# Kernel tuning notes

Measured on AMD Instinct MI355X. Metric: run time of the kernel, lower is better.

## Reference

```python
import jax, jax.numpy as jnp
import numpy as np

B, S, H, I, E, K = 2, 512, 1024, 4096, 8, 2
LN_EPS = 1e-5


def setup_inputs() -> dict:
    key = jax.random.key(0)
    ks = jax.random.split(key, 5)
    sc = 0.02  # init scale for weights
    return {
        "hidden_states": jax.random.normal(ks[0], (B, S, H), jnp.float32),
        "ln_w": jnp.ones((H,), jnp.float32),
        "ln_b": jnp.zeros((H,), jnp.float32),
        "Wr": jax.random.normal(ks[1], (E, H), jnp.float32) * sc,  # router [out=E, in=H]
        "br": jnp.zeros((E,), jnp.float32),
        "W1": jax.random.normal(ks[2], (E, I, H), jnp.float32) * sc,  # dense1 per expert [out=I, in=H]
        "b1": jnp.zeros((E, I), jnp.float32),
        "W2": jax.random.normal(ks[3], (E, H, I), jnp.float32) * sc,  # dense2 per expert [out=H, in=I]
        "b2": jnp.zeros((E, H), jnp.float32),
    }


def reference(hidden_states, ln_w, ln_b, Wr, br, W1, b1, W2, b2):
    # Eval mode: no jitter noise, no dropout.
    residual = hidden_states
    mu = jnp.mean(hidden_states, axis=-1, keepdims=True)
    var = jnp.mean(jnp.square(hidden_states - mu), axis=-1, keepdims=True)
    x = (hidden_states - mu) * jax.lax.rsqrt(var + LN_EPS) * ln_w + ln_b  # [B,S,H]

    logits = jnp.einsum("bsh,eh->bse", x, Wr) + br  # [B,S,E]
    topw, topi = jax.lax.top_k(logits, K)  # [B,S,K]
    topw = jax.nn.softmax(topw, axis=-1)
    # Combine weights per expert (top-k indices are distinct, so scatter == first-match)
    combine = jnp.sum(jax.nn.one_hot(topi, E, dtype=x.dtype) * topw[..., None], axis=-2)  # [B,S,E]

    # Dense per-expert FFN (reference form of gather-FFN-scatter); combine zeros out unselected experts
    a = jax.nn.gelu(jnp.einsum("bsh,eih->bsei", x, W1) + b1, approximate=False)  # [B,S,E,I]
    y = jnp.einsum("bsei,ehi->bseh", a, W2) + b2  # [B,S,E,H]
    out = residual + jnp.einsum("bse,bseh->bsh", combine, y)

    probs = jax.nn.softmax(logits, axis=-1)
    usage = jnp.mean(probs, axis=(0, 1))  # [E]
    balance_loss = E * jnp.sum(usage * usage) - 1.0
    return out, balance_loss
```

## Files before the change

### kernel.cpp

```cpp
#include <hip/hip_runtime.h>
#include <hip/hip_bf16.h>
#include <math.h>
#include <stdint.h>

#define T_TOK 1024
#define H_DIM 1024
#define I_DIM 4096
#define E_NUM 8
#define NSLOT (2 * T_TOK)
#define WELEM 33554432

typedef __attribute__((ext_vector_type(8))) short bf16x8;
typedef __attribute__((ext_vector_type(4))) float f32x4;

#define MFMA_BF16(a, b, c) __builtin_amdgcn_mfma_f32_16x16x32_bf16(a, b, c, 0, 0, 0)

__device__ __forceinline__ short f2bf(float f) {
  union { float f; unsigned u; } x; x.f = f;
  unsigned r = (x.u + 0x7fffu + ((x.u >> 16) & 1u)) >> 16;
  return (short)r;
}
__device__ __forceinline__ int pack2bf(float a, float b) {
  return ((int)(unsigned short)f2bf(a)) | (((int)f2bf(b)) << 16);
}

typedef __attribute__((address_space(3))) unsigned int as3_u32;
typedef const __attribute__((address_space(1))) unsigned int as1_u32c;
__device__ __forceinline__ void glds16(const void* g, void* l) {
  __builtin_amdgcn_global_load_lds((as1_u32c*)g, (as3_u32*)l, 16, 0, 0);
}

union BBCast { int4 i4; bf16x8 v; };

__global__ __launch_bounds__(256) void k_ln_router(
    const float* __restrict__ x, const float* __restrict__ ln_w,
    const float* __restrict__ ln_b, const float* __restrict__ Wr,
    const float* __restrict__ br,
    short* __restrict__ xln, int* __restrict__ sel_e, float* __restrict__ sel_w,
    float* __restrict__ probs, float* __restrict__ out) {
  const int t = blockIdx.x;
  const int tid = threadIdx.x;
  const int lane = tid & 63, wid = tid >> 6;
  __shared__ float sx[H_DIM];
  __shared__ float redS[8];
  __shared__ float slog[E_NUM];

  float4 v = ((const float4*)(x + (size_t)t * H_DIM))[tid];
  ((float4*)(out + (size_t)t * H_DIM))[tid] = v;
  float s = v.x + v.y + v.z + v.w;
  float ss = v.x * v.x + v.y * v.y + v.z * v.z + v.w * v.w;
  for (int o = 32; o > 0; o >>= 1) { s += __shfl_down(s, o); ss += __shfl_down(ss, o); }
  if (lane == 0) { redS[wid] = s; redS[4 + wid] = ss; }
  __syncthreads();
  float st = redS[0] + redS[1] + redS[2] + redS[3];
  float sst = redS[4] + redS[5] + redS[6] + redS[7];
  float mu = st * (1.0f / H_DIM);
  float var = sst * (1.0f / H_DIM) - mu * mu;
  float rs = rsqrtf(var + 1e-5f);

  float4 lw = ((const float4*)ln_w)[tid];
  float4 lb = ((const float4*)ln_b)[tid];
  float4 xn;
  xn.x = (v.x - mu) * rs * lw.x + lb.x;
  xn.y = (v.y - mu) * rs * lw.y + lb.y;
  xn.z = (v.z - mu) * rs * lw.z + lb.z;
  xn.w = (v.w - mu) * rs * lw.w + lb.w;
  sx[4 * tid + 0] = xn.x; sx[4 * tid + 1] = xn.y;
  sx[4 * tid + 2] = xn.z; sx[4 * tid + 3] = xn.w;
  short4 s4;
  s4.x = f2bf(xn.x); s4.y = f2bf(xn.y); s4.z = f2bf(xn.z); s4.w = f2bf(xn.w);
  ((short4*)(xln + (size_t)t * H_DIM))[tid] = s4;
  __syncthreads();

  for (int e = 2 * wid; e < 2 * wid + 2; ++e) {
    float p = 0.f;
    for (int h = lane; h < H_DIM; h += 64) p += sx[h] * Wr[e * H_DIM + h];
    for (int o = 32; o > 0; o >>= 1) p += __shfl_down(p, o);
    if (lane == 0) slog[e] = p + br[e];
  }
  __syncthreads();

  if (tid == 0) {
    float lg[E_NUM];
    for (int e = 0; e < E_NUM; ++e) lg[e] = slog[e];
    int i0 = 0;
    for (int e = 1; e < E_NUM; ++e) if (lg[e] > lg[i0]) i0 = e;
    int i1 = (i0 == 0) ? 1 : 0;
    for (int e = 0; e < E_NUM; ++e) if (e != i0 && lg[e] > lg[i1]) i1 = e;
    float w1e = __expf(lg[i1] - lg[i0]);
    float den = 1.f + w1e;
    sel_e[2 * t] = i0; sel_w[2 * t] = 1.f / den;
    sel_e[2 * t + 1] = i1; sel_w[2 * t + 1] = w1e / den;
    float se = 0.f, pe[E_NUM];
    for (int e = 0; e < E_NUM; ++e) { pe[e] = __expf(lg[e] - lg[i0]); se += pe[e]; }
    float inv = 1.f / se;
    for (int e = 0; e < E_NUM; ++e) probs[t * E_NUM + e] = pe[e] * inv;
  }
}

__global__ __launch_bounds__(512) void k_route(
    const int* __restrict__ sel_e, const float* __restrict__ sel_w,
    const float* __restrict__ probs,
    int* __restrict__ counts, int* __restrict__ basep,
    int* __restrict__ tlist, int* __restrict__ sel_idx,
    float* __restrict__ wslot, float* __restrict__ loss_out) {
  const int wid = threadIdx.x >> 6;
  const int lane = threadIdx.x & 63;
  __shared__ int scnt[E_NUM];
  __shared__ float susage[E_NUM];

  int cnt = 0;
  for (int s0 = 0; s0 < NSLOT; s0 += 64) {
    int s = s0 + lane;
    bool m = (sel_e[s] == wid);
    unsigned long long mk = __ballot(m);
    int pre = __popcll(mk & ((1ULL << lane) - 1ULL));
    if (m) {
      int idx = cnt + pre;
      sel_idx[s] = idx;
      tlist[wid * T_TOK + idx] = s >> 1;
      wslot[wid * T_TOK + idx] = sel_w[s];
    }
    cnt += __popcll(mk);
  }
  if (lane == 0) scnt[wid] = cnt;

  float u = 0.f;
  for (int t = lane; t < T_TOK; t += 64) u += probs[t * E_NUM + wid];
  for (int o = 32; o > 0; o >>= 1) u += __shfl_down(u, o);
  if (lane == 0) susage[wid] = u * (1.0f / T_TOK);
  __syncthreads();

  if (threadIdx.x == 0) {
    int b = 0;
    for (int e = 0; e < E_NUM; ++e) { basep[e] = b; counts[e] = scnt[e]; b += scnt[e]; }
    float sq = 0.f;
    for (int e = 0; e < E_NUM; ++e) sq += susage[e] * susage[e];
    *loss_out = (float)E_NUM * sq - 1.0f;
  }
}

__global__ __launch_bounds__(256) void k_cvt(const float* __restrict__ src,
                                             short* __restrict__ dst, int n) {
  const int stride = gridDim.x * blockDim.x;
  for (int i = blockIdx.x * blockDim.x + threadIdx.x; i < (n >> 3); i += stride) {
    float4 a = ((const float4*)src)[2 * i];
    float4 b = ((const float4*)src)[2 * i + 1];
    int4 p;
    p.x = pack2bf(a.x, a.y); p.y = pack2bf(a.z, a.w);
    p.z = pack2bf(b.x, b.y); p.w = pack2bf(b.z, b.w);
    ((int4*)dst)[i] = p;
  }
}

__global__ __launch_bounds__(256) void k_ffn1(
    const short* __restrict__ xln, const short* __restrict__ W1b,
    const float* __restrict__ b1, const int* __restrict__ counts,
    const int* __restrict__ basep, const int* __restrict__ tlist,
    short* __restrict__ a_buf) {
  const int e = blockIdx.z;
  const int cnt = counts[e];
  const int m0 = blockIdx.y * 128;
  if (m0 >= cnt) return;
  const int n0 = blockIdx.x * 128;

  __shared__ __align__(16) short As[3][128 * 32];
  __shared__ __align__(16) short Bs[3][128 * 32];

  const int tid = threadIdx.x;
  const int lane = tid & 63, wid = tid >> 6;
  const int wr = wid >> 1, wc = wid & 1;
  const int fr = lane & 15, fq = lane >> 4;

  int r0 = m0 + (tid >> 2); if (r0 >= cnt) r0 = cnt - 1;
  int r1 = m0 + 64 + (tid >> 2); if (r1 >= cnt) r1 = cnt - 1;
  const short* ag0 = xln + (size_t)tlist[e * T_TOK + r0] * H_DIM + (tid & 3) * 8;
  const short* ag1 = xln + (size_t)tlist[e * T_TOK + r1] * H_DIM + (tid & 3) * 8;
  const short* bg0 = W1b + ((size_t)e * I_DIM + n0 + (tid >> 2)) * H_DIM + (tid & 3) * 8;
  const short* bg1 = bg0 + (size_t)64 * H_DIM;

  f32x4 acc[4][4];
#pragma unroll
  for (int i = 0; i < 4; ++i)
#pragma unroll
    for (int j = 0; j < 4; ++j) acc[i][j] = (f32x4)0.f;

#define STAGE(kk, buf)                                  \
  {                                                     \
    glds16(ag0 + (kk), &As[buf][tid * 8]);              \
    glds16(ag1 + (kk), &As[buf][(256 + tid) * 8]);      \
    glds16(bg0 + (kk), &Bs[buf][tid * 8]);              \
    glds16(bg1 + (kk), &Bs[buf][(256 + tid) * 8]);      \
  }

  STAGE(0, 0);
  STAGE(32, 1);

  const int KT = H_DIM / 32;
  for (int kt = 0; kt < KT; ++kt) {
    if (kt == KT - 1) {
      asm volatile("s_waitcnt vmcnt(0)" ::: "memory");
    } else {
      asm volatile("s_waitcnt vmcnt(4)" ::: "memory");
    }
    __builtin_amdgcn_s_barrier();
    if (kt + 2 < KT) STAGE((kt + 2) * 32, (kt + 2) % 3);
    const int cb = kt % 3;
    bf16x8 af[4], bb[4];
#pragma unroll
    for (int mi = 0; mi < 4; ++mi)
      af[mi] = *(const bf16x8*)&As[cb][(wr * 64 + mi * 16 + fr) * 32 + fq * 8];
#pragma unroll
    for (int ni = 0; ni < 4; ++ni)
      bb[ni] = *(const bf16x8*)&Bs[cb][(wc * 64 + ni * 16 + fr) * 32 + fq * 8];
#pragma unroll
    for (int mi = 0; mi < 4; ++mi)
#pragma unroll
      for (int ni = 0; ni < 4; ++ni)
        acc[mi][ni] = MFMA_BF16(af[mi], bb[ni], acc[mi][ni]);
  }
#undef STAGE

  const int slot0 = basep[e] + m0;
  float b1v[4];
#pragma unroll
  for (int ni = 0; ni < 4; ++ni)
    b1v[ni] = b1[e * I_DIM + n0 + wc * 64 + ni * 16 + fr];
#pragma unroll
  for (int mi = 0; mi < 4; ++mi)
#pragma unroll
    for (int j = 0; j < 4; ++j) {
      int r = wr * 64 + mi * 16 + fq * 4 + j;
      if (m0 + r < cnt) {
        size_t rowoff = (size_t)(slot0 + r) * I_DIM;
#pragma unroll
        for (int ni = 0; ni < 4; ++ni) {
          int colg = n0 + wc * 64 + ni * 16 + fr;
          float vv = acc[mi][ni][j] + b1v[ni];
          float g = 0.5f * vv * (1.0f + erff(vv * 0.70710678118654752f));
          a_buf[rowoff + colg] = f2bf(g);
        }
      }
    }
}

__global__ __launch_bounds__(256) void k_ffn2(
    const short* __restrict__ a_buf, const short* __restrict__ W2b,
    const float* __restrict__ b2, const int* __restrict__ counts,
    const int* __restrict__ basep, const int* __restrict__ tlist,
    const float* __restrict__ wslot, float* __restrict__ out) {
  const int z = blockIdx.z;
  const int e = z >> 2;
  const int kc = z & 3;
  const int CH = I_DIM / 4;
  const int cnt = counts[e];
  const int m0 = blockIdx.y * 128;
  if (m0 >= cnt) return;
  const int n0 = blockIdx.x * 128;

  __shared__ __align__(16) short As[3][128 * 32];
  __shared__ __align__(16) short Bs[3][128 * 32];

  const int tid = threadIdx.x;
  const int lane = tid & 63, wid = tid >> 6;
  const int wr = wid >> 1, wc = wid & 1;
  const int fr = lane & 15, fq = lane >> 4;

  int r0 = m0 + (tid >> 2); if (r0 >= cnt) r0 = cnt - 1;
  int r1 = m0 + 64 + (tid >> 2); if (r1 >= cnt) r1 = cnt - 1;
  const int sb = basep[e];
  const short* ag0 = a_buf + (size_t)(sb + r0) * I_DIM + kc * CH + (tid & 3) * 8;
  const short* ag1 = a_buf + (size_t)(sb + r1) * I_DIM + kc * CH + (tid & 3) * 8;
  const short* bg0 = W2b + ((size_t)e * H_DIM + n0 + (tid >> 2)) * I_DIM + kc * CH + (tid & 3) * 8;
  const short* bg1 = bg0 + (size_t)64 * I_DIM;

  f32x4 acc[4][4];
#pragma unroll
  for (int i = 0; i < 4; ++i)
#pragma unroll
    for (int j = 0; j < 4; ++j) acc[i][j] = (f32x4)0.f;

#define STAGE(kk, buf)                                  \
  {                                                     \
    glds16(ag0 + (kk), &As[buf][tid * 8]);              \
    glds16(ag1 + (kk), &As[buf][(256 + tid) * 8]);      \
    glds16(bg0 + (kk), &Bs[buf][tid * 8]);              \
    glds16(bg1 + (kk), &Bs[buf][(256 + tid) * 8]);      \
  }

  STAGE(0, 0);
  STAGE(32, 1);

  const int KT = CH / 32;
  for (int kt = 0; kt < KT; ++kt) {
    if (kt == KT - 1) {
      asm volatile("s_waitcnt vmcnt(0)" ::: "memory");
    } else {
      asm volatile("s_waitcnt vmcnt(4)" ::: "memory");
    }
    __builtin_amdgcn_s_barrier();
    if (kt + 2 < KT) STAGE((kt + 2) * 32, (kt + 2) % 3);
    const int cb = kt % 3;
    bf16x8 af[4], bb[4];
#pragma unroll
    for (int mi = 0; mi < 4; ++mi)
      af[mi] = *(const bf16x8*)&As[cb][(wr * 64 + mi * 16 + fr) * 32 + fq * 8];
#pragma unroll
    for (int ni = 0; ni < 4; ++ni)
      bb[ni] = *(const bf16x8*)&Bs[cb][(wc * 64 + ni * 16 + fr) * 32 + fq * 8];
#pragma unroll
    for (int mi = 0; mi < 4; ++mi)
#pragma unroll
      for (int ni = 0; ni < 4; ++ni)
        acc[mi][ni] = MFMA_BF16(af[mi], bb[ni], acc[mi][ni]);
  }
#undef STAGE

  float b2v[4];
#pragma unroll
  for (int ni = 0; ni < 4; ++ni)
    b2v[ni] = 0.25f * b2[e * H_DIM + n0 + wc * 64 + ni * 16 + fr];
#pragma unroll
  for (int mi = 0; mi < 4; ++mi)
#pragma unroll
    for (int j = 0; j < 4; ++j) {
      int r = wr * 64 + mi * 16 + fq * 4 + j;
      if (m0 + r < cnt) {
        int tok = tlist[e * T_TOK + m0 + r];
        float w = wslot[e * T_TOK + m0 + r];
        float* orow = out + (size_t)tok * H_DIM;
#pragma unroll
        for (int ni = 0; ni < 4; ++ni) {
          int colg = n0 + wc * 64 + ni * 16 + fr;
          atomicAdd(&orow[colg], w * (acc[mi][ni][j] + b2v[ni]));
        }
      }
    }
}

__global__ __launch_bounds__(256) void k_ffn1_f32(
    const short* __restrict__ xln, const float* __restrict__ W1,
    const float* __restrict__ b1, const int* __restrict__ counts,
    const int* __restrict__ basep, const int* __restrict__ tlist,
    short* __restrict__ a_buf) {
  const int e = blockIdx.z;
  const int cnt = counts[e];
  const int m0 = blockIdx.y * 128;
  if (m0 >= cnt) return;
  const int n0 = blockIdx.x * 128;
  __shared__ __align__(16) short As[2][128 * 32];
  __shared__ __align__(16) float Bsf[2][128 * 32];
  const int tid = threadIdx.x;
  const int lane = tid & 63, wid = tid >> 6;
  const int wr = wid >> 1, wc = wid & 1;
  const int fr = lane & 15, fq = lane >> 4;
  int r0 = m0 + (tid >> 2); if (r0 >= cnt) r0 = cnt - 1;
  int r1 = m0 + 64 + (tid >> 2); if (r1 >= cnt) r1 = cnt - 1;
  const short* ag0 = xln + (size_t)tlist[e * T_TOK + r0] * H_DIM + (tid & 3) * 8;
  const short* ag1 = xln + (size_t)tlist[e * T_TOK + r1] * H_DIM + (tid & 3) * 8;
  const int bro = tid >> 3;
  const int bslot = (tid & 7) ^ (bro & 7);
  const float* bg = W1 + ((size_t)e * I_DIM + n0 + bro) * H_DIM + bslot * 4;
  f32x4 acc[4][4];
#pragma unroll
  for (int i = 0; i < 4; ++i)
#pragma unroll
    for (int j = 0; j < 4; ++j) acc[i][j] = (f32x4)0.f;
#define STAGE(kk, buf)                                                      \
  {                                                                         \
    glds16(ag0 + (kk), &As[buf][tid * 8]);                                  \
    glds16(ag1 + (kk), &As[buf][(256 + tid) * 8]);                          \
    _Pragma("unroll") for (int i = 0; i < 4; ++i)                           \
        glds16(bg + (size_t)(i * 32) * H_DIM + (kk),                        \
               &Bsf[buf][(i * 256 + tid) * 4]);                             \
  }
  STAGE(0, 0);
  __syncthreads();
  int cur = 0;
  for (int kt = 0; kt < H_DIM / 32; ++kt) {
    if (kt + 1 < H_DIM / 32) STAGE((kt + 1) * 32, cur ^ 1);
    bf16x8 af[4], bb[4];
#pragma unroll
    for (int mi = 0; mi < 4; ++mi)
      af[mi] = *(const bf16x8*)&As[cur][(wr * 64 + mi * 16 + fr) * 32 + fq * 8];
#pragma unroll
    for (int ni = 0; ni < 4; ++ni) {
      const int row = wc * 64 + ni * 16 + fr;
      const int base = row * 128 + fq * 32;
      const int sw = (row & 7) << 4;
      f32x4 lo = *(const f32x4*)((const char*)&Bsf[cur][0] + (base ^ sw));
      f32x4 hi = *(const f32x4*)((const char*)&Bsf[cur][0] + ((base + 16) ^ sw));
      BBCast c;
      c.i4.x = pack2bf(lo[0], lo[1]); c.i4.y = pack2bf(lo[2], lo[3]);
      c.i4.z = pack2bf(hi[0], hi[1]); c.i4.w = pack2bf(hi[2], hi[3]);
      bb[ni] = c.v;
    }
#pragma unroll
    for (int mi = 0; mi < 4; ++mi)
#pragma unroll
      for (int ni = 0; ni < 4; ++ni)
        acc[mi][ni] = MFMA_BF16(af[mi], bb[ni], acc[mi][ni]);
    __syncthreads();
    cur ^= 1;
  }
#undef STAGE
  const int slot0 = basep[e] + m0;
  float b1v[4];
#pragma unroll
  for (int ni = 0; ni < 4; ++ni)
    b1v[ni] = b1[e * I_DIM + n0 + wc * 64 + ni * 16 + fr];
#pragma unroll
  for (int mi = 0; mi < 4; ++mi)
#pragma unroll
    for (int j = 0; j < 4; ++j) {
      int r = wr * 64 + mi * 16 + fq * 4 + j;
      if (m0 + r < cnt) {
        size_t rowoff = (size_t)(slot0 + r) * I_DIM;
#pragma unroll
        for (int ni = 0; ni < 4; ++ni) {
          int colg = n0 + wc * 64 + ni * 16 + fr;
          float vv = acc[mi][ni][j] + b1v[ni];
          float g = 0.5f * vv * (1.0f + erff(vv * 0.70710678118654752f));
          a_buf[rowoff + colg] = f2bf(g);
        }
      }
    }
}

__global__ __launch_bounds__(256) void k_ffn2_f32(
    const short* __restrict__ a_buf, const float* __restrict__ W2,
    const float* __restrict__ b2, const int* __restrict__ counts,
    const int* __restrict__ basep, const int* __restrict__ tlist,
    const float* __restrict__ wslot, float* __restrict__ out, int lg) {
  const int z = blockIdx.z;
  const int e = z >> lg;
  const int kc = z & ((1 << lg) - 1);
  const int CH = I_DIM >> lg;
  const int cnt = counts[e];
  const int m0 = blockIdx.y * 128;
  if (m0 >= cnt) return;
  const int n0 = blockIdx.x * 128;
  __shared__ __align__(16) short As[2][128 * 32];
  __shared__ __align__(16) float Bsf[2][128 * 32];
  const int tid = threadIdx.x;
  const int lane = tid & 63, wid = tid >> 6;
  const int wr = wid >> 1, wc = wid & 1;
  const int fr = lane & 15, fq = lane >> 4;
  int r0 = m0 + (tid >> 2); if (r0 >= cnt) r0 = cnt - 1;
  int r1 = m0 + 64 + (tid >> 2); if (r1 >= cnt) r1 = cnt - 1;
  const int sb = basep[e];
  const short* ag0 = a_buf + (size_t)(sb + r0) * I_DIM + kc * CH + (tid & 3) * 8;
  const short* ag1 = a_buf + (size_t)(sb + r1) * I_DIM + kc * CH + (tid & 3) * 8;
  const int bro = tid >> 3;
  const int bslot = (tid & 7) ^ (bro & 7);
  const float* bg = W2 + ((size_t)e * H_DIM + n0 + bro) * I_DIM + kc * CH + bslot * 4;
  f32x4 acc[4][4];
#pragma unroll
  for (int i = 0; i < 4; ++i)
#pragma unroll
    for (int j = 0; j < 4; ++j) acc[i][j] = (f32x4)0.f;
#define STAGE(kk, buf)                                                      \
  {                                                                         \
    glds16(ag0 + (kk), &As[buf][tid * 8]);                                  \
    glds16(ag1 + (kk), &As[buf][(256 + tid) * 8]);                          \
    _Pragma("unroll") for (int i = 0; i < 4; ++i)                           \
        glds16(bg + (size_t)(i * 32) * I_DIM + (kk),                        \
               &Bsf[buf][(i * 256 + tid) * 4]);                             \
  }
  STAGE(0, 0);
  __syncthreads();
  const int KT = CH / 32;
  int cur = 0;
  for (int kt = 0; kt < KT; ++kt) {
    if (kt + 1 < KT) STAGE((kt + 1) * 32, cur ^ 1);
    bf16x8 af[4], bb[4];
#pragma unroll
    for (int mi = 0; mi < 4; ++mi)
      af[mi] = *(const bf16x8*)&As[cur][(wr * 64 + mi * 16 + fr) * 32 + fq * 8];
#pragma unroll
    for (int ni = 0; ni < 4; ++ni) {
      const int row = wc * 64 + ni * 16 + fr;
      const int base = row * 128 + fq * 32;
      const int sw = (row & 7) << 4;
      f32x4 lo = *(const f32x4*)((const char*)&Bsf[cur][0] + (base ^ sw));
      f32x4 hi = *(const f32x4*)((const char*)&Bsf[cur][0] + ((base + 16) ^ sw));
      BBCast c;
      c.i4.x = pack2bf(lo[0], lo[1]); c.i4.y = pack2bf(lo[2], lo[3]);
      c.i4.z = pack2bf(hi[0], hi[1]); c.i4.w = pack2bf(hi[2], hi[3]);
      bb[ni] = c.v;
    }
#pragma unroll
    for (int mi = 0; mi < 4; ++mi)
#pragma unroll
      for (int ni = 0; ni < 4; ++ni)
        acc[mi][ni] = MFMA_BF16(af[mi], bb[ni], acc[mi][ni]);
    __syncthreads();
    cur ^= 1;
  }
#undef STAGE
  const float inv = 1.0f / (float)(1 << lg);
  float b2v[4];
#pragma unroll
  for (int ni = 0; ni < 4; ++ni)
    b2v[ni] = inv * b2[e * H_DIM + n0 + wc * 64 + ni * 16 + fr];
#pragma unroll
  for (int mi = 0; mi < 4; ++mi)
#pragma unroll
    for (int j = 0; j < 4; ++j) {
      int r = wr * 64 + mi * 16 + fq * 4 + j;
      if (m0 + r < cnt) {
        int tok = tlist[e * T_TOK + m0 + r];
        float w = wslot[e * T_TOK + m0 + r];
        float* orow = out + (size_t)tok * H_DIM;
#pragma unroll
        for (int ni = 0; ni < 4; ++ni) {
          int colg = n0 + wc * 64 + ni * 16 + fr;
          atomicAdd(&orow[colg], w * (acc[mi][ni][j] + b2v[ni]));
        }
      }
    }
}

extern "C" void kernel_launch(void* const* d_in, const int* in_sizes, int n_in,
                              void* d_out, int out_size, void* d_ws, size_t ws_size,
                              hipStream_t stream) {
  const float* hidden = (const float*)d_in[0];
  const float* ln_w = (const float*)d_in[1];
  const float* ln_b = (const float*)d_in[2];
  const float* Wr = (const float*)d_in[3];
  const float* br = (const float*)d_in[4];
  const float* W1 = (const float*)d_in[5];
  const float* b1 = (const float*)d_in[6];
  const float* W2 = (const float*)d_in[7];
  const float* b2 = (const float*)d_in[8];
  float* out = (float*)d_out;

  char* w = (char*)d_ws;
  int* counts = (int*)(w + 0);
  int* basep = (int*)(w + 256);
  float* probs = (float*)(w + 512);
  int* tlist = (int*)(w + 33280);
  int* sel_e = (int*)(w + 66048);
  int* sel_idx = (int*)(w + 74240);
  float* sel_w = (float*)(w + 82432);
  float* wslot = (float*)(w + 90624);
  short* xln = (short*)(w + 131072);
  short* a_buf = (short*)(w + 2228224);
  short* w_bf = (short*)(w + 19005440);
  const size_t REQ_NEW = 19005440 + (size_t)WELEM * 2;

  k_ln_router<<<T_TOK, 256, 0, stream>>>(hidden, ln_w, ln_b, Wr, br, xln,
                                         sel_e, sel_w, probs, out);
  k_route<<<1, 512, 0, stream>>>(sel_e, sel_w, probs, counts, basep, tlist,
                                 sel_idx, wslot, out + (size_t)T_TOK * H_DIM);

  if (ws_size >= REQ_NEW) {
    k_cvt<<<2048, 256, 0, stream>>>(W1, w_bf, WELEM);
    k_ffn1<<<dim3(I_DIM / 128, T_TOK / 128, E_NUM), 256, 0, stream>>>(
        xln, w_bf, b1, counts, basep, tlist, a_buf);
    k_cvt<<<2048, 256, 0, stream>>>(W2, w_bf, WELEM);
    k_ffn2<<<dim3(H_DIM / 128, T_TOK / 128, E_NUM * 4), 256, 0, stream>>>(
        a_buf, w_bf, b2, counts, basep, tlist, wslot, out);
  } else {
    const int lg = 2;
    k_ffn1_f32<<<dim3(I_DIM / 128, T_TOK / 128, E_NUM), 256, 0, stream>>>(
        xln, W1, b1, counts, basep, tlist, a_buf);
    k_ffn2_f32<<<dim3(H_DIM / 128, T_TOK / 128, E_NUM << lg), 256, 0, stream>>>(
        a_buf, W2, b2, counts, basep, tlist, wslot, out, lg);
  }
}
```

Baseline: 249.4 us.

## Pre-tile bf16 weights and activations, overlap weight conversion with other kernels

Weight conversion to bf16 now writes a tiled 128x32 layout so GEMM tiles load as contiguous 8KB chunks. The per-expert activation buffer uses the same layout, with each expert's slot base padded to 128 rows. W1 conversion is folded into the layernorm/router kernel as extra blocks, and W2 conversion runs as extra z-slices of the ffn1 grid when the workspace is large enough. This removes separate conversion launches and lets conversion overlap compute, but it needs a larger workspace, and if the workspace is too small it falls back to a sequential path or to the fp32 kernels.

```diff
diff --git a/kernel.cpp b/kernel.cpp
--- a/kernel.cpp
+++ b/kernel.cpp
@@ -32,18 +32,48 @@
 
 union BBCast { int4 i4; bf16x8 v; };
 
-__global__ __launch_bounds__(256) void k_ln_router(
+__device__ __forceinline__ void cvtpack_dev(const float* __restrict__ src,
+                                            short* __restrict__ dst,
+                                            int bid, int nb, int rsh, int csh) {
+  const size_t total8 = ((size_t)E_NUM << (rsh + csh)) >> 3;
+  const int kmask = (1 << (csh - 3)) - 1;
+  const int nmask = (1 << rsh) - 1;
+  for (size_t id = (size_t)bid * 256 + threadIdx.x; id < total8;
+       id += (size_t)nb * 256) {
+    int k8 = (int)(id & kmask);
+    int n = (int)((id >> (csh - 3)) & nmask);
+    int e = (int)(id >> (csh - 3 + rsh));
+    int k = k8 << 3;
+    size_t eoff = (size_t)e << (rsh + csh);
+    const float* s = src + eoff + ((size_t)n << csh) + k;
+    float4 a = *(const float4*)s;
+    float4 b = *(const float4*)(s + 4);
+    int4 p;
+    p.x = pack2bf(a.x, a.y); p.y = pack2bf(a.z, a.w);
+    p.z = pack2bf(b.x, b.y); p.w = pack2bf(b.z, b.w);
+    size_t tile = ((size_t)(n >> 7) << (csh - 5)) + (k >> 5);
+    *(int4*)(dst + eoff + tile * 4096 + ((n & 127) << 5) + (k & 31)) = p;
+  }
+}
+
+__global__ __launch_bounds__(256) void k_pre(
     const float* __restrict__ x, const float* __restrict__ ln_w,
     const float* __restrict__ ln_b, const float* __restrict__ Wr,
     const float* __restrict__ br,
     short* __restrict__ xln, int* __restrict__ sel_e, float* __restrict__ sel_w,
-    float* __restrict__ probs, float* __restrict__ out) {
+    float* __restrict__ probs, float* __restrict__ out,
+    const float* __restrict__ W1src, short* __restrict__ w1dst, int ncvt) {
+  __shared__ float sx[H_DIM];
+  __shared__ float redS[8];
+  __shared__ float slog[E_NUM];
+
+  if (blockIdx.x >= T_TOK) {
+    cvtpack_dev(W1src, w1dst, blockIdx.x - T_TOK, ncvt, 12, 10);
+    return;
+  }
   const int t = blockIdx.x;
   const int tid = threadIdx.x;
   const int lane = tid & 63, wid = tid >> 6;
-  __shared__ float sx[H_DIM];
-  __shared__ float redS[8];
-  __shared__ float slog[E_NUM];
 
   float4 v = ((const float4*)(x + (size_t)t * H_DIM))[tid];
   ((float4*)(out + (size_t)t * H_DIM))[tid] = v;
@@ -133,31 +163,35 @@
 
   if (threadIdx.x == 0) {
     int b = 0;
-    for (int e = 0; e < E_NUM; ++e) { basep[e] = b; counts[e] = scnt[e]; b += scnt[e]; }
+    for (int e = 0; e < E_NUM; ++e) {
+      basep[e] = b; counts[e] = scnt[e];
+      b += (scnt[e] + 127) & ~127;
+    }
     float sq = 0.f;
     for (int e = 0; e < E_NUM; ++e) sq += susage[e] * susage[e];
     *loss_out = (float)E_NUM * sq - 1.0f;
   }
 }
 
-__global__ __launch_bounds__(256) void k_cvt(const float* __restrict__ src,
-                                             short* __restrict__ dst, int n) {
-  const int stride = gridDim.x * blockDim.x;
-  for (int i = blockIdx.x * blockDim.x + threadIdx.x; i < (n >> 3); i += stride) {
-    float4 a = ((const float4*)src)[2 * i];
-    float4 b = ((const float4*)src)[2 * i + 1];
-    int4 p;
-    p.x = pack2bf(a.x, a.y); p.y = pack2bf(a.z, a.w);
-    p.z = pack2bf(b.x, b.y); p.w = pack2bf(b.z, b.w);
-    ((int4*)dst)[i] = p;
-  }
+__global__ __launch_bounds__(256) void k_cvtpack(const float* __restrict__ src,
+                                                 short* __restrict__ dst,
+                                                 int rsh, int csh) {
+  cvtpack_dev(src, dst, blockIdx.x, gridDim.x, rsh, csh);
 }
 
 __global__ __launch_bounds__(256) void k_ffn1(
     const short* __restrict__ xln, const short* __restrict__ W1b,
     const float* __restrict__ b1, const int* __restrict__ counts,
     const int* __restrict__ basep, const int* __restrict__ tlist,
-    short* __restrict__ a_buf) {
+    short* __restrict__ a_buf,
+    const float* __restrict__ W2src, short* __restrict__ w2dst) {
+  if (blockIdx.z >= E_NUM) {
+    int cb = (blockIdx.z - E_NUM) * gridDim.x * gridDim.y +
+             blockIdx.y * gridDim.x + blockIdx.x;
+    int nb = (gridDim.z - E_NUM) * gridDim.x * gridDim.y;
+    cvtpack_dev(W2src, w2dst, cb, nb, 10, 12);
+    return;
+  }
   const int e = blockIdx.z;
   const int cnt = counts[e];
   const int m0 = blockIdx.y * 128;
@@ -176,8 +210,7 @@
   int r1 = m0 + 64 + (tid >> 2); if (r1 >= cnt) r1 = cnt - 1;
   const short* ag0 = xln + (size_t)tlist[e * T_TOK + r0] * H_DIM + (tid & 3) * 8;
   const short* ag1 = xln + (size_t)tlist[e * T_TOK + r1] * H_DIM + (tid & 3) * 8;
-  const short* bg0 = W1b + ((size_t)e * I_DIM + n0 + (tid >> 2)) * H_DIM + (tid & 3) * 8;
-  const short* bg1 = bg0 + (size_t)64 * H_DIM;
+  const short* bgp = W1b + ((size_t)e << 22) + ((size_t)(n0 >> 7) * 131072) + tid * 8;
 
   f32x4 acc[4][4];
 #pragma unroll
@@ -185,16 +218,17 @@
 #pragma unroll
     for (int j = 0; j < 4; ++j) acc[i][j] = (f32x4)0.f;
 
-#define STAGE(kk, buf)                                  \
-  {                                                     \
-    glds16(ag0 + (kk), &As[buf][tid * 8]);              \
-    glds16(ag1 + (kk), &As[buf][(256 + tid) * 8]);      \
-    glds16(bg0 + (kk), &Bs[buf][tid * 8]);              \
-    glds16(bg1 + (kk), &Bs[buf][(256 + tid) * 8]);      \
+#define STAGE(kt, buf)                                          \
+  {                                                             \
+    glds16(ag0 + (kt) * 32, &As[buf][tid * 8]);                 \
+    glds16(ag1 + (kt) * 32, &As[buf][(256 + tid) * 8]);         \
+    glds16(bgp + (size_t)(kt) * 4096, &Bs[buf][tid * 8]);       \
+    glds16(bgp + (size_t)(kt) * 4096 + 2048,                    \
+           &Bs[buf][(256 + tid) * 8]);                          \
   }
 
   STAGE(0, 0);
-  STAGE(32, 1);
+  STAGE(1, 1);
 
   const int KT = H_DIM / 32;
   for (int kt = 0; kt < KT; ++kt) {
@@ -204,7 +238,7 @@
       asm volatile("s_waitcnt vmcnt(4)" ::: "memory");
     }
     __builtin_amdgcn_s_barrier();
-    if (kt + 2 < KT) STAGE((kt + 2) * 32, (kt + 2) % 3);
+    if (kt + 2 < KT) STAGE(kt + 2, (kt + 2) % 3);
     const int cb = kt % 3;
     bf16x8 af[4], bb[4];
 #pragma unroll
@@ -221,7 +255,8 @@
   }
 #undef STAGE
 
-  const int slot0 = basep[e] + m0;
+  const size_t T1 = (size_t)(basep[e] + m0) >> 7;
+  short* abase = a_buf + T1 * 524288;
   float b1v[4];
 #pragma unroll
   for (int ni = 0; ni < 4; ++ni)
@@ -232,13 +267,12 @@
     for (int j = 0; j < 4; ++j) {
       int r = wr * 64 + mi * 16 + fq * 4 + j;
       if (m0 + r < cnt) {
-        size_t rowoff = (size_t)(slot0 + r) * I_DIM;
 #pragma unroll
         for (int ni = 0; ni < 4; ++ni) {
           int colg = n0 + wc * 64 + ni * 16 + fr;
           float vv = acc[mi][ni][j] + b1v[ni];
           float g = 0.5f * vv * (1.0f + erff(vv * 0.70710678118654752f));
-          a_buf[rowoff + colg] = f2bf(g);
+          abase[(size_t)(colg >> 5) * 4096 + r * 32 + (colg & 31)] = f2bf(g);
         }
       }
     }
@@ -252,7 +286,6 @@
   const int z = blockIdx.z;
   const int e = z >> 2;
   const int kc = z & 3;
-  const int CH = I_DIM / 4;
   const int cnt = counts[e];
   const int m0 = blockIdx.y * 128;
   if (m0 >= cnt) return;
@@ -266,13 +299,10 @@
   const int wr = wid >> 1, wc = wid & 1;
   const int fr = lane & 15, fq = lane >> 4;
 
-  int r0 = m0 + (tid >> 2); if (r0 >= cnt) r0 = cnt - 1;
-  int r1 = m0 + 64 + (tid >> 2); if (r1 >= cnt) r1 = cnt - 1;
-  const int sb = basep[e];
-  const short* ag0 = a_buf + (size_t)(sb + r0) * I_DIM + kc * CH + (tid & 3) * 8;
-  const short* ag1 = a_buf + (size_t)(sb + r1) * I_DIM + kc * CH + (tid & 3) * 8;
-  const short* bg0 = W2b + ((size_t)e * H_DIM + n0 + (tid >> 2)) * I_DIM + kc * CH + (tid & 3) * 8;
-  const short* bg1 = bg0 + (size_t)64 * I_DIM;
+  const size_t T1 = (size_t)(basep[e] + m0) >> 7;
+  const short* agp = a_buf + T1 * 524288 + (size_t)kc * 131072 + tid * 8;
+  const short* bgp = W2b + ((size_t)e << 22) + ((size_t)(n0 >> 7) * 524288) +
+                     (size_t)kc * 131072 + tid * 8;
 
   f32x4 acc[4][4];
 #pragma unroll
@@ -280,18 +310,20 @@
 #pragma unroll
     for (int j = 0; j < 4; ++j) acc[i][j] = (f32x4)0.f;
 
-#define STAGE(kk, buf)                                  \
-  {                                                     \
-    glds16(ag0 + (kk), &As[buf][tid * 8]);              \
-    glds16(ag1 + (kk), &As[buf][(256 + tid) * 8]);      \
-    glds16(bg0 + (kk), &Bs[buf][tid * 8]);              \
-    glds16(bg1 + (kk), &Bs[buf][(256 + tid) * 8]);      \
+#define STAGE(kt, buf)                                          \
+  {                                                             \
+    glds16(agp + (size_t)(kt) * 4096, &As[buf][tid * 8]);       \
+    glds16(agp + (size_t)(kt) * 4096 + 2048,                    \
+           &As[buf][(256 + tid) * 8]);                          \
+    glds16(bgp + (size_t)(kt) * 4096, &Bs[buf][tid * 8]);       \
+    glds16(bgp + (size_t)(kt) * 4096 + 2048,                    \
+           &Bs[buf][(256 + tid) * 8]);                          \
   }
 
   STAGE(0, 0);
-  STAGE(32, 1);
-
-  const int KT = CH / 32;
+  STAGE(1, 1);
+
+  const int KT = 32;
   for (int kt = 0; kt < KT; ++kt) {
     if (kt == KT - 1) {
       asm volatile("s_waitcnt vmcnt(0)" ::: "memory");
@@ -299,7 +331,7 @@
       asm volatile("s_waitcnt vmcnt(4)" ::: "memory");
     }
     __builtin_amdgcn_s_barrier();
-    if (kt + 2 < KT) STAGE((kt + 2) * 32, (kt + 2) % 3);
+    if (kt + 2 < KT) STAGE(kt + 2, (kt + 2) % 3);
     const int cb = kt % 3;
     bf16x8 af[4], bb[4];
 #pragma unroll
@@ -546,22 +578,33 @@
   float* wslot = (float*)(w + 90624);
   short* xln = (short*)(w + 131072);
   short* a_buf = (short*)(w + 2228224);
-  short* w_bf = (short*)(w + 19005440);
-  const size_t REQ_NEW = 19005440 + (size_t)WELEM * 2;
-
-  k_ln_router<<<T_TOK, 256, 0, stream>>>(hidden, ln_w, ln_b, Wr, br, xln,
-                                         sel_e, sel_w, probs, out);
-  k_route<<<1, 512, 0, stream>>>(sel_e, sel_w, probs, counts, basep, tlist,
-                                 sel_idx, wslot, out + (size_t)T_TOK * H_DIM);
-
-  if (ws_size >= REQ_NEW) {
-    k_cvt<<<2048, 256, 0, stream>>>(W1, w_bf, WELEM);
-    k_ffn1<<<dim3(I_DIM / 128, T_TOK / 128, E_NUM), 256, 0, stream>>>(
-        xln, w_bf, b1, counts, basep, tlist, a_buf);
-    k_cvt<<<2048, 256, 0, stream>>>(W2, w_bf, WELEM);
+  short* w1_bf = (short*)(w + 27394048);
+  short* w2_bf = (short*)(w + 94502912);
+  const size_t REQ_SEQ = 94502912;
+  const size_t REQ_FUSED = 161611776;
+
+  if (ws_size >= REQ_SEQ) {
+    const bool fused = (ws_size >= REQ_FUSED);
+    short* w2dst = fused ? w2_bf : w1_bf;
+    k_pre<<<T_TOK + 1024, 256, 0, stream>>>(hidden, ln_w, ln_b, Wr, br, xln,
+                                            sel_e, sel_w, probs, out, W1, w1_bf, 1024);
+    k_route<<<1, 512, 0, stream>>>(sel_e, sel_w, probs, counts, basep, tlist,
+                                   sel_idx, wslot, out + (size_t)T_TOK * H_DIM);
+    if (fused) {
+      k_ffn1<<<dim3(I_DIM / 128, T_TOK / 128, E_NUM + 4), 256, 0, stream>>>(
+          xln, w1_bf, b1, counts, basep, tlist, a_buf, W2, w2_bf);
+    } else {
+      k_ffn1<<<dim3(I_DIM / 128, T_TOK / 128, E_NUM), 256, 0, stream>>>(
+          xln, w1_bf, b1, counts, basep, tlist, a_buf, nullptr, nullptr);
+      k_cvtpack<<<1024, 256, 0, stream>>>(W2, w2dst, 10, 12);
+    }
     k_ffn2<<<dim3(H_DIM / 128, T_TOK / 128, E_NUM * 4), 256, 0, stream>>>(
-        a_buf, w_bf, b2, counts, basep, tlist, wslot, out);
+        a_buf, w2dst, b2, counts, basep, tlist, wslot, out);
   } else {
+    k_pre<<<T_TOK, 256, 0, stream>>>(hidden, ln_w, ln_b, Wr, br, xln,
+                                     sel_e, sel_w, probs, out, nullptr, nullptr, 0);
+    k_route<<<1, 512, 0, stream>>>(sel_e, sel_w, probs, counts, basep, tlist,
+                                   sel_idx, wslot, out + (size_t)T_TOK * H_DIM);
     const int lg = 2;
     k_ffn1_f32<<<dim3(I_DIM / 128, T_TOK / 128, E_NUM), 256, 0, stream>>>(
         xln, W1, b1, counts, basep, tlist, a_buf);
```

Measured after the change: 229.1 us. -8.1%, faster.
